# Kernel optimization log

Measured on AMD Instinct MI355X. Metric: run time of the kernel, lower is better.

Reference implementation:

```python
import jax, jax.numpy as jnp
import numpy as np

EPS = 1e-6
LAMB = 0.05
NEG = -1000.0


def setup_inputs() -> dict:
    key = jax.random.key(0)
    k1, k2, k3, k4, k5, k6 = jax.random.split(key, 6)
    Bi, Bt, K, L, D = 128, 128, 36, 64, 1024
    imgs = jax.random.normal(k1, (Bi, K, D), dtype=jnp.float32)
    caps = jax.random.normal(k2, (Bt, L, D), dtype=jnp.float32)
    img_cls = jax.random.normal(k3, (Bi, D), dtype=jnp.float32)
    cap_cls = jax.random.normal(k4, (Bt, D), dtype=jnp.float32)
    # variable lengths; pin one element to max so torch's [:, :max] slice is identity
    img_lens = jax.random.randint(k5, (Bi,), K // 2, K + 1).astype(jnp.int32).at[0].set(K)
    cap_lens = jax.random.randint(k6, (Bt,), L // 2, L + 1).astype(jnp.int32).at[0].set(L)
    return {"img_cls": img_cls, "imgs": imgs, "cap_cls": cap_cls,
            "caps": caps, "img_lens": img_lens, "cap_lens": cap_lens}


def reference(img_cls, imgs, cap_cls, caps, img_lens, cap_lens):
    # HiCHAN.forward_cam (img_cls / cap_cls unused by this branch)
    imgs = imgs + EPS
    caps = caps + EPS
    imgs = imgs / jnp.linalg.norm(imgs, axis=-1, keepdims=True)
    caps = caps / jnp.linalg.norm(caps, axis=-1, keepdims=True)

    K, L = imgs.shape[1], caps.shape[1]
    # fine-grained similarity tensor [Bi, Bt, K, L]
    fg_sims = jnp.einsum('ikd,tld->itkl', imgs, caps)

    # fg mask: valid region k of image i AND valid word l of caption t
    img_valid = jnp.arange(K)[None, :] < img_lens[:, None]      # [Bi, K]
    cap_valid = jnp.arange(L)[None, :] < cap_lens[:, None]      # [Bt, L]
    mask = img_valid[:, None, :, None] & cap_valid[None, :, None, :]  # [Bi,Bt,K,L] bool
    m = mask.astype(fg_sims.dtype)

    # masked temperature softmax (single scores tensor reused for both axes)
    scores = jnp.where(mask, fg_sims, NEG) / LAMB
    v2t_attn = jax.nn.softmax(scores, axis=-1)
    v2t = jnp.sum(v2t_attn * fg_sims * m, axis=-1)   # [Bi,Bt,K]
    t2v_attn = jax.nn.softmax(scores, axis=-2)
    t2v = jnp.sum(t2v_attn * fg_sims * m, axis=-2)   # [Bi,Bt,L]

    # _ave_init: uniform weights over valid rows / cols
    r_b = mask.any(axis=-1).astype(fg_sims.dtype)    # [Bi,Bt,K]
    c_b = mask.any(axis=-2).astype(fg_sims.dtype)    # [Bi,Bt,L]
    r = r_b / r_b.sum(axis=-1, keepdims=True)
    c = c_b / c_b.sum(axis=-1, keepdims=True)

    sims = (jnp.sum(v2t * r, axis=-1) + jnp.sum(t2v * c, axis=-1)) / 2  # [Bi,Bt]
    return sims
```

## Files before the change

kernel.cpp:

```cpp
#include <hip/hip_runtime.h>
#include <stdint.h>

#define BI 128
#define BT 128
#define KIMG 36
#define LCAP 64
#define DD 1024
#define MP 48
#define MB 96
#define NB 256
#define ABUF 6144

typedef _Float16 h4 __attribute__((ext_vector_type(4)));
typedef _Float16 h8 __attribute__((ext_vector_type(8)));
typedef float f4 __attribute__((ext_vector_type(4)));

__device__ __forceinline__ float wave_red_sum(float v) {
#pragma unroll
  for (int o = 1; o < 64; o <<= 1) v += __shfl_xor(v, o, 64);
  return v;
}
__device__ __forceinline__ float wave_red_max(float v) {
#pragma unroll
  for (int o = 1; o < 64; o <<= 1) v = fmaxf(v, __shfl_xor(v, o, 64));
  return v;
}

__global__ __launch_bounds__(256) void norm_kernel(
    const float* __restrict__ imgs, const float* __restrict__ caps,
    _Float16* __restrict__ Ah, _Float16* __restrict__ Bh) {
  int lane = threadIdx.x & 63;
  int wv = threadIdx.x >> 6;
  int row = blockIdx.x * 4 + wv;
  const float* src;
  bool isCap;
  int r = 0;
  if (row < BI * MP) {
    int i = row / MP, k = row - i * MP;
    isCap = false;
    if (k >= KIMG) {
      h4 z = {};
#pragma unroll
      for (int seg = 0; seg < 4; ++seg)
        ((h4*)(Ah + (size_t)row * DD))[lane + 64 * seg] = z;
      return;
    }
    src = imgs + ((size_t)i * KIMG + k) * DD;
  } else {
    r = row - BI * MP;
    isCap = true;
    src = caps + (size_t)r * DD;
  }
  float4 x[4];
  float ss = 0.f;
#pragma unroll
  for (int seg = 0; seg < 4; ++seg) {
    x[seg] = ((const float4*)src)[lane + 64 * seg];
    x[seg].x += 1e-6f; x[seg].y += 1e-6f; x[seg].z += 1e-6f; x[seg].w += 1e-6f;
    ss += x[seg].x * x[seg].x + x[seg].y * x[seg].y +
          x[seg].z * x[seg].z + x[seg].w * x[seg].w;
  }
  ss = wave_red_sum(ss);
  float scale = rsqrtf(ss);
#pragma unroll
  for (int seg = 0; seg < 4; ++seg) {
    h4 o;
    o[0] = (_Float16)(x[seg].x * scale);
    o[1] = (_Float16)(x[seg].y * scale);
    o[2] = (_Float16)(x[seg].z * scale);
    o[3] = (_Float16)(x[seg].w * scale);
    if (!isCap) {
      ((h4*)(Ah + (size_t)row * DD))[lane + 64 * seg] = o;
    } else {
      int k = 4 * (lane + 64 * seg);
      size_t tile = (size_t)(r >> 4) * 32 + (k >> 5);
      int sub = ((k >> 3) & 3) * 128 + (r & 15) * 8 + (k & 7);
      *(h4*)(Bh + tile * 512 + sub) = o;
    }
  }
}

__global__ __launch_bounds__(256, 3) void sims_kernel(
    const _Float16* __restrict__ Ah, const _Float16* __restrict__ Bh,
    const int* __restrict__ img_lens, const int* __restrict__ cap_lens,
    float* __restrict__ out) {
  __shared__ char stage[2 * ABUF] __attribute__((aligned(16)));

  int tid = threadIdx.x;
  int lane = tid & 63;
  int w = tid >> 6;

  int wgid = blockIdx.x;
  int xcd = wgid & 7;
  int slot = wgid >> 3;
  int bx = 4 * xcd + (slot & 3);
  int by = slot >> 2;

  int fr = lane & 15;
  int fq = lane >> 4;

  const size_t arow0 = (size_t)by * MB;

  const int c0 = (w < 2) ? 2 * w : w + 2;
  const int nch = (w < 2) ? 2 : 1;
  int s0 = c0 * 64 + lane;
  int sw0 = s0 ^ ((s0 >> 3) & 7);
  const _Float16* gpA = Ah + (arow0 + (sw0 >> 2)) * DD + (sw0 & 3) * 8;
  const int lds0 = c0 * 1024 + lane * 16;

  int sl = 4 * fr + fq;
  const int aoff0 = (sl ^ ((sl >> 3) & 7)) * 16;

  const _Float16* bp[4];
#pragma unroll
  for (int ni = 0; ni < 4; ++ni)
    bp[ni] = Bh + ((size_t)((bx * 16) + 4 * w + ni) * 32) * 512 + lane * 8;

  f4 acc[6][4] = {};
  h8 bfA[4], bfB[4];

  auto STAGE = [&](int buf, int k0) {
    __builtin_amdgcn_global_load_lds(
        (const __attribute__((address_space(1))) void*)(gpA + k0),
        (__attribute__((address_space(3))) void*)(stage + buf * ABUF + lds0), 16, 0, 0);
    if (nch == 2)
      __builtin_amdgcn_global_load_lds(
          (const __attribute__((address_space(1))) void*)(gpA + 16 * DD + k0),
          (__attribute__((address_space(3))) void*)(stage + buf * ABUF + lds0 + 1024), 16, 0, 0);
  };
  auto LOADB = [&](h8(&bf)[4], int t) {
#pragma unroll
    for (int ni = 0; ni < 4; ++ni) bf[ni] = *(const h8*)(bp[ni] + 512 * t);
  };
  auto BODY = [&](int t, int parity, h8(&cur)[4], h8(&nxt)[4]) {
    if (t < 31) {
      STAGE(parity ^ 1, 32 * (t + 1));
      LOADB(nxt, t + 1);
    }
    const char* rb = stage + parity * ABUF;
    h8 af[6];
#pragma unroll
    for (int mi = 0; mi < 6; ++mi)
      af[mi] = *(const h8*)(rb + aoff0 + 1024 * mi);
    __builtin_amdgcn_s_setprio(1);
#pragma unroll
    for (int mi = 0; mi < 6; ++mi)
#pragma unroll
      for (int ni = 0; ni < 4; ++ni)
        acc[mi][ni] = __builtin_amdgcn_mfma_f32_16x16x32_f16(
            af[mi], cur[ni], acc[mi][ni], 0, 0, 0);
    __builtin_amdgcn_s_setprio(0);
    __syncthreads();
  };

  STAGE(0, 0);
  LOADB(bfA, 0);
  __syncthreads();

  for (int tt = 0; tt < 32; tt += 2) {
    BODY(tt, 0, bfA, bfB);
    BODY(tt + 1, 1, bfB, bfA);
  }

  int t = bx * 4 + w;
  int Lt = cap_lens[t];

#pragma unroll
  for (int img = 0; img < 2; ++img) {
    int Ki = img_lens[2 * by + img];

    float m = -1e30f;
#pragma unroll
    for (int mi = 0; mi < 3; ++mi)
#pragma unroll
      for (int ni = 0; ni < 4; ++ni)
#pragma unroll
        for (int j = 0; j < 4; ++j) {
          bool valid = (16 * mi + 4 * fq + j < Ki) && (16 * ni + fr < Lt);
          if (valid) m = fmaxf(m, acc[3 * img + mi][ni][j]);
        }
    m = wave_red_max(m);

    float rowe[3][4] = {}, rowes[3][4] = {}, cole[4] = {}, coles[4] = {};
#pragma unroll
    for (int mi = 0; mi < 3; ++mi)
#pragma unroll
      for (int ni = 0; ni < 4; ++ni)
#pragma unroll
        for (int j = 0; j < 4; ++j) {
          float s = acc[3 * img + mi][ni][j];
          bool valid = (16 * mi + 4 * fq + j < Ki) && (16 * ni + fr < Lt);
          float e = valid ? __expf((s - m) * 20.0f) : 0.f;
          float es = e * s;
          rowe[mi][j] += e;
          rowes[mi][j] += es;
          cole[ni] += e;
          coles[ni] += es;
        }

    float part = 0.f;
#pragma unroll
    for (int mi = 0; mi < 3; ++mi)
#pragma unroll
      for (int j = 0; j < 4; ++j) {
        float Re = rowe[mi][j], Res = rowes[mi][j];
#pragma unroll
        for (int o = 1; o < 16; o <<= 1) {
          Re += __shfl_xor(Re, o, 64);
          Res += __shfl_xor(Res, o, 64);
        }
        int row = 16 * mi + 4 * fq + j;
        if (fr == 0 && row < Ki) part += (Res / Re) * (0.5f / (float)Ki);
      }
#pragma unroll
    for (int ni = 0; ni < 4; ++ni) {
      float Ce = cole[ni], Ces = coles[ni];
#pragma unroll
      for (int o = 16; o < 64; o <<= 1) {
        Ce += __shfl_xor(Ce, o, 64);
        Ces += __shfl_xor(Ces, o, 64);
      }
      int l = 16 * ni + fr;
      if (fq == 0 && l < Lt) part += (Ces / Ce) * (0.5f / (float)Lt);
    }
    float sim = wave_red_sum(part);
    if (lane == 0) out[(size_t)(2 * by + img) * BT + t] = sim;
  }
}

extern "C" void kernel_launch(void* const* d_in, const int* in_sizes, int n_in,
                              void* d_out, int out_size, void* d_ws, size_t ws_size,
                              hipStream_t stream) {
  const float* imgs = (const float*)d_in[1];
  const float* caps = (const float*)d_in[3];
  const int* img_lens = (const int*)d_in[4];
  const int* cap_lens = (const int*)d_in[5];
  float* out = (float*)d_out;

  _Float16* Ah = (_Float16*)d_ws;
  _Float16* Bh = Ah + (size_t)BI * MP * DD;

  norm_kernel<<<(BI * MP + BT * LCAP) / 4, 256, 0, stream>>>(imgs, caps, Ah, Bh);
  sims_kernel<<<2048, 256, 0, stream>>>(Ah, Bh, img_lens, cap_lens, out);
}
```

Baseline: 132.5 us.

## Pre-swizzle A into MFMA fragment layout and load both operands directly to registers

The normalization kernel now writes both the image and caption fp16 matrices in a tiled, MFMA-fragment-ordered layout, grouped so each workgroup's K-step tiles are contiguous. The sims kernel drops the LDS staging of A and its per-step barriers, and instead double-buffers A and B fragments straight from global memory into registers. This removes LDS traffic and synchronisation, but each wave now loads the shared A tile separately, which raises global/L2 read traffic and register pressure.

```diff
diff --git a/kernel.cpp b/kernel.cpp
--- a/kernel.cpp
+++ b/kernel.cpp
@@ -7,9 +7,6 @@
 #define LCAP 64
 #define DD 1024
 #define MP 48
-#define MB 96
-#define NB 256
-#define ABUF 6144
 
 typedef _Float16 h4 __attribute__((ext_vector_type(4)));
 typedef _Float16 h8 __attribute__((ext_vector_type(8)));
@@ -28,64 +25,74 @@
 
 __global__ __launch_bounds__(256) void norm_kernel(
     const float* __restrict__ imgs, const float* __restrict__ caps,
-    _Float16* __restrict__ Ah, _Float16* __restrict__ Bh) {
+    _Float16* __restrict__ Afm, _Float16* __restrict__ Bfm) {
   int lane = threadIdx.x & 63;
   int wv = threadIdx.x >> 6;
   int row = blockIdx.x * 4 + wv;
-  const float* src;
-  bool isCap;
-  int r = 0;
+
+  const float* src = nullptr;
+  _Float16* base;
+  int rr;
+  size_t tile0;
+  int tstride;
+  bool zero = false;
+
   if (row < BI * MP) {
-    int i = row / MP, k = row - i * MP;
-    isCap = false;
-    if (k >= KIMG) {
-      h4 z = {};
-#pragma unroll
-      for (int seg = 0; seg < 4; ++seg)
-        ((h4*)(Ah + (size_t)row * DD))[lane + 64 * seg] = z;
-      return;
-    }
-    src = imgs + ((size_t)i * KIMG + k) * DD;
+    int i = row / MP, kr = row - i * MP;
+    int p = i >> 1;
+    int row96 = (i & 1) * MP + kr;
+    int rt = row96 >> 4;
+    rr = row96 & 15;
+    tile0 = (size_t)(p * 32) * 6 + rt;
+    tstride = 6;
+    base = Afm;
+    if (kr >= KIMG) zero = true;
+    else src = imgs + ((size_t)i * KIMG + kr) * DD;
   } else {
-    r = row - BI * MP;
-    isCap = true;
+    int r = row - BI * MP;
+    int cap = r >> 6, word = r & 63;
+    int bx = cap >> 2;
+    int ct = (cap & 3) * 4 + (word >> 4);
+    rr = word & 15;
+    tile0 = (size_t)(bx * 32) * 16 + ct;
+    tstride = 16;
+    base = Bfm;
     src = caps + (size_t)r * DD;
   }
+
   float4 x[4];
   float ss = 0.f;
+  if (!zero) {
+#pragma unroll
+    for (int seg = 0; seg < 4; ++seg) {
+      x[seg] = ((const float4*)src)[lane + 64 * seg];
+      x[seg].x += 1e-6f; x[seg].y += 1e-6f; x[seg].z += 1e-6f; x[seg].w += 1e-6f;
+      ss += x[seg].x * x[seg].x + x[seg].y * x[seg].y +
+            x[seg].z * x[seg].z + x[seg].w * x[seg].w;
+    }
+    ss = wave_red_sum(ss);
+  }
+  float scale = zero ? 0.f : rsqrtf(ss);
 #pragma unroll
   for (int seg = 0; seg < 4; ++seg) {
-    x[seg] = ((const float4*)src)[lane + 64 * seg];
-    x[seg].x += 1e-6f; x[seg].y += 1e-6f; x[seg].z += 1e-6f; x[seg].w += 1e-6f;
-    ss += x[seg].x * x[seg].x + x[seg].y * x[seg].y +
-          x[seg].z * x[seg].z + x[seg].w * x[seg].w;
-  }
-  ss = wave_red_sum(ss);
-  float scale = rsqrtf(ss);
-#pragma unroll
-  for (int seg = 0; seg < 4; ++seg) {
-    h4 o;
-    o[0] = (_Float16)(x[seg].x * scale);
-    o[1] = (_Float16)(x[seg].y * scale);
-    o[2] = (_Float16)(x[seg].z * scale);
-    o[3] = (_Float16)(x[seg].w * scale);
-    if (!isCap) {
-      ((h4*)(Ah + (size_t)row * DD))[lane + 64 * seg] = o;
-    } else {
-      int k = 4 * (lane + 64 * seg);
-      size_t tile = (size_t)(r >> 4) * 32 + (k >> 5);
-      int sub = ((k >> 3) & 3) * 128 + (r & 15) * 8 + (k & 7);
-      *(h4*)(Bh + tile * 512 + sub) = o;
+    h4 o = {};
+    if (!zero) {
+      o[0] = (_Float16)(x[seg].x * scale);
+      o[1] = (_Float16)(x[seg].y * scale);
+      o[2] = (_Float16)(x[seg].z * scale);
+      o[3] = (_Float16)(x[seg].w * scale);
     }
+    int k = 4 * (lane + 64 * seg);
+    int t = k >> 5, kk = k & 31;
+    int sub = ((kk >> 3) * 16 + rr) * 8 + (kk & 7);
+    *(h4*)(base + (tile0 + (size_t)t * tstride) * 512 + sub) = o;
   }
 }
 
 __global__ __launch_bounds__(256, 3) void sims_kernel(
-    const _Float16* __restrict__ Ah, const _Float16* __restrict__ Bh,
+    const _Float16* __restrict__ Afm, const _Float16* __restrict__ Bfm,
     const int* __restrict__ img_lens, const int* __restrict__ cap_lens,
     float* __restrict__ out) {
-  __shared__ char stage[2 * ABUF] __attribute__((aligned(16)));
-
   int tid = threadIdx.x;
   int lane = tid & 63;
   int w = tid >> 6;
@@ -99,68 +106,47 @@
   int fr = lane & 15;
   int fq = lane >> 4;
 
-  const size_t arow0 = (size_t)by * MB;
-
-  const int c0 = (w < 2) ? 2 * w : w + 2;
-  const int nch = (w < 2) ? 2 : 1;
-  int s0 = c0 * 64 + lane;
-  int sw0 = s0 ^ ((s0 >> 3) & 7);
-  const _Float16* gpA = Ah + (arow0 + (sw0 >> 2)) * DD + (sw0 & 3) * 8;
-  const int lds0 = c0 * 1024 + lane * 16;
-
-  int sl = 4 * fr + fq;
-  const int aoff0 = (sl ^ ((sl >> 3) & 7)) * 16;
-
-  const _Float16* bp[4];
-#pragma unroll
-  for (int ni = 0; ni < 4; ++ni)
-    bp[ni] = Bh + ((size_t)((bx * 16) + 4 * w + ni) * 32) * 512 + lane * 8;
+  const _Float16* ap = Afm + ((size_t)(by * 32) * 6) * 512 + lane * 8;
+  const _Float16* bp = Bfm + ((size_t)(bx * 32) * 16 + w * 4) * 512 + lane * 8;
 
   f4 acc[6][4] = {};
-  h8 bfA[4], bfB[4];
-
-  auto STAGE = [&](int buf, int k0) {
-    __builtin_amdgcn_global_load_lds(
-        (const __attribute__((address_space(1))) void*)(gpA + k0),
-        (__attribute__((address_space(3))) void*)(stage + buf * ABUF + lds0), 16, 0, 0);
-    if (nch == 2)
-      __builtin_amdgcn_global_load_lds(
-          (const __attribute__((address_space(1))) void*)(gpA + 16 * DD + k0),
-          (__attribute__((address_space(3))) void*)(stage + buf * ABUF + lds0 + 1024), 16, 0, 0);
+  h8 afA[6], afB[6], bfA[4], bfB[4];
+
+  auto LOADA = [&](h8(&af)[6], int t) {
+#pragma unroll
+    for (int mi = 0; mi < 6; ++mi)
+      af[mi] = *(const h8*)(ap + (size_t)(t * 6 + mi) * 512);
   };
   auto LOADB = [&](h8(&bf)[4], int t) {
 #pragma unroll
-    for (int ni = 0; ni < 4; ++ni) bf[ni] = *(const h8*)(bp[ni] + 512 * t);
+    for (int ni = 0; ni < 4; ++ni)
+      bf[ni] = *(const h8*)(bp + (size_t)(t * 16 + ni) * 512);
   };
-  auto BODY = [&](int t, int parity, h8(&cur)[4], h8(&nxt)[4]) {
-    if (t < 31) {
-      STAGE(parity ^ 1, 32 * (t + 1));
-      LOADB(nxt, t + 1);
-    }
-    const char* rb = stage + parity * ABUF;
-    h8 af[6];
-#pragma unroll
-    for (int mi = 0; mi < 6; ++mi)
-      af[mi] = *(const h8*)(rb + aoff0 + 1024 * mi);
+  auto MFMA = [&](h8(&af)[6], h8(&bf)[4]) {
     __builtin_amdgcn_s_setprio(1);
 #pragma unroll
     for (int mi = 0; mi < 6; ++mi)
 #pragma unroll
       for (int ni = 0; ni < 4; ++ni)
         acc[mi][ni] = __builtin_amdgcn_mfma_f32_16x16x32_f16(
-            af[mi], cur[ni], acc[mi][ni], 0, 0, 0);
+            af[mi], bf[ni], acc[mi][ni], 0, 0, 0);
     __builtin_amdgcn_s_setprio(0);
-    __syncthreads();
   };
 
-  STAGE(0, 0);
+  LOADA(afA, 0);
   LOADB(bfA, 0);
-  __syncthreads();
-
-  for (int tt = 0; tt < 32; tt += 2) {
-    BODY(tt, 0, bfA, bfB);
-    BODY(tt + 1, 1, bfB, bfA);
-  }
+  for (int tt = 0; tt < 30; tt += 2) {
+    LOADA(afB, tt + 1);
+    LOADB(bfB, tt + 1);
+    MFMA(afA, bfA);
+    LOADA(afA, tt + 2);
+    LOADB(bfA, tt + 2);
+    MFMA(afB, bfB);
+  }
+  LOADA(afB, 31);
+  LOADB(bfB, 31);
+  MFMA(afA, bfA);
+  MFMA(afB, bfB);
 
   int t = bx * 4 + w;
   int Lt = cap_lens[t];
@@ -237,9 +223,9 @@
   const int* cap_lens = (const int*)d_in[5];
   float* out = (float*)d_out;
 
-  _Float16* Ah = (_Float16*)d_ws;
-  _Float16* Bh = Ah + (size_t)BI * MP * DD;
-
-  norm_kernel<<<(BI * MP + BT * LCAP) / 4, 256, 0, stream>>>(imgs, caps, Ah, Bh);
-  sims_kernel<<<2048, 256, 0, stream>>>(Ah, Bh, img_lens, cap_lens, out);
-}
+  _Float16* Afm = (_Float16*)d_ws;
+  _Float16* Bfm = Afm + (size_t)BI * MP * DD;
+
+  norm_kernel<<<(BI * MP + BT * LCAP) / 4, 256, 0, stream>>>(imgs, caps, Afm, Bfm);
+  sims_kernel<<<2048, 256, 0, stream>>>(Afm, Bfm, img_lens, cap_lens, out);
+}
```

Result: slower. 284.0 us (+114.3%).
